# Performance work log

Hardware: AMD Instinct MI355X
Metric: run time of the kernel (lower is better)

The kernel has to match this reference:

```python
import jax, jax.numpy as jnp
import numpy as np

B, N, FEAT = 64, 1024, 3
HID, STATE, LAYERS, NTYPES = 64, 32, 2, 10


def setup_inputs() -> dict:
    key = jax.random.key(0)
    ks = jax.random.split(key, 16)
    s = 0.1
    return {
        "task_features": jax.random.normal(ks[0], (B, N, FEAT), jnp.float32),
        "task_types": jax.random.randint(ks[1], (B, N), 0, NTYPES, jnp.int32),
        "prev_state": jnp.zeros((B, STATE), jnp.float32),
        "enc_w1": jax.random.normal(ks[2], (HID, FEAT), jnp.float32) * s,
        "enc_b1": jnp.zeros((HID,), jnp.float32),
        "enc_w2": jax.random.normal(ks[3], (HID, HID), jnp.float32) * s,
        "enc_b2": jnp.zeros((HID,), jnp.float32),
        "contention": jax.random.normal(ks[4], (NTYPES, NTYPES), jnp.float32) * 0.1,
        "gnn_w": jax.random.normal(ks[5], (LAYERS, HID, HID), jnp.float32) * s,
        "gnn_b": jnp.zeros((LAYERS, HID), jnp.float32),
        "gru_w_ih": jax.random.normal(ks[6], (3 * STATE, HID), jnp.float32) * s,
        "gru_w_hh": jax.random.normal(ks[7], (3 * STATE, STATE), jnp.float32) * s,
        "gru_b_ih": jnp.zeros((3 * STATE,), jnp.float32),
        "gru_b_hh": jnp.zeros((3 * STATE,), jnp.float32),
        "head_w1": jax.random.normal(ks[8], (HID, HID + STATE), jnp.float32) * s,
        "head_b1": jnp.zeros((HID,), jnp.float32),
        "head_w2": jax.random.normal(ks[9], (1, HID), jnp.float32) * s,
        "head_b2": jnp.zeros((1,), jnp.float32),
    }


def _forward(task_features, task_types, prev_state, enc_w1, enc_b1, enc_w2, enc_b2,
             contention, gnn_w, gnn_b, gru_w_ih, gru_w_hh, gru_b_ih, gru_b_hh,
             head_w1, head_b1, head_w2, head_b2):
    # task encoder: Linear -> ReLU -> Linear
    emb = jax.nn.relu(task_features @ enc_w1.T + enc_b1) @ enc_w2.T + enc_b2  # (B,N,H)
    # interaction graph: type-pair gather + cosine similarity
    base = contention[task_types[:, :, None], task_types[:, None, :]]  # (B,N,N)
    nrm = emb / jnp.maximum(jnp.linalg.norm(emb, axis=-1, keepdims=True), 1e-12)
    sim = jnp.einsum("bnd,bmd->bnm", nrm, nrm)
    adjacency = jax.nn.sigmoid(base) * sim  # (B,N,N)
    # GNN layers: aggregate + linear + relu
    h = emb
    for l in range(LAYERS):
        agg = jnp.einsum("bnm,bmd->bnd", adjacency, h)
        h = jax.nn.relu((h + agg) @ gnn_w[l].T + gnn_b[l])
    ctx = h.mean(axis=1)  # (B,H)
    # GRUCell (torch semantics)
    gi = ctx @ gru_w_ih.T + gru_b_ih
    gh = prev_state @ gru_w_hh.T + gru_b_hh
    i_r, i_z, i_n = jnp.split(gi, 3, axis=-1)
    h_r, h_z, h_n = jnp.split(gh, 3, axis=-1)
    r = jax.nn.sigmoid(i_r + h_r)
    z = jax.nn.sigmoid(i_z + h_z)
    n = jnp.tanh(i_n + r * h_n)
    new_state = (1.0 - z) * n + z * prev_state  # (B,S)
    # latency head on [h, state]
    st = jnp.broadcast_to(new_state[:, None, :], (h.shape[0], h.shape[1], new_state.shape[-1]))
    combined = jnp.concatenate([h, st], axis=-1)
    lat = jax.nn.relu(combined @ head_w1.T + head_b1) @ head_w2.T + head_b2
    return lat[..., 0], new_state


def reference(task_features, task_types, prev_state, enc_w1, enc_b1, enc_w2, enc_b2,
              contention, gnn_w, gnn_b, gru_w_ih, gru_w_hh, gru_b_ih, gru_b_hh,
              head_w1, head_b1, head_w2, head_b2):
    return _forward(task_features, task_types, prev_state, enc_w1, enc_b1, enc_w2, enc_b2,
                    contention, gnn_w, gnn_b, gru_w_ih, gru_w_hh, gru_b_ih, gru_b_hh,
                    head_w1, head_b1, head_w2, head_b2)
```

## Files before the change

kernel.cpp:

```cpp
#include <hip/hip_runtime.h>
#include <math.h>

#define BB 64
#define NN 1024
#define HID 64
#define STATE 32
#define NTYPES 10
#define CAP 256
#define CAPE (CAP * 64)

typedef _Float16 f16;
typedef f16 f16x8 __attribute__((ext_vector_type(8)));
typedef f16 f16x4 __attribute__((ext_vector_type(4)));
typedef float f32x4 __attribute__((ext_vector_type(4)));

#define MFMA16(a, b, c) __builtin_amdgcn_mfma_f32_16x16x32_f16(a, b, c, 0, 0, 0)

__device__ __forceinline__ float sigm(float x) { return 1.f / (1.f + expf(-x)); }

__device__ __forceinline__ f16x8 cvt8(float4 a, float4 b) {
    f16x8 r;
    r[0] = (f16)a.x; r[1] = (f16)a.y; r[2] = (f16)a.z; r[3] = (f16)a.w;
    r[4] = (f16)b.x; r[5] = (f16)b.y; r[6] = (f16)b.z; r[7] = (f16)b.w;
    return r;
// ... 2 lines not shown
    union { f16 h[2]; unsigned u; } p;
    p.h[0] = a; p.h[1] = b;
    return p.u;
}

__device__ __forceinline__ void swz_load(const float* __restrict__ W, int K, int n,
                                         f16* dst, int tid) {
    for (int p = tid; p < n; p += 256) {
        int j = p & 7, ln = (p >> 3) & 63, nt = (p >> 9) & 3, ch = p >> 11;
        int k = ch * 32 + ((ln >> 4) << 3) + j;
        int o = nt * 16 + (ln & 15);
        dst[p] = (f16)W[o * K + k];
    }
}

__global__ __launch_bounds__(256) void k_encoder(
    const float* __restrict__ feat,
    const float* __restrict__ w1, const float* __restrict__ b1,
    const float* __restrict__ w2, const float* __restrict__ b2,
    const int* __restrict__ types, int* __restrict__ idx, int* __restrict__ cnt,
    f16* __restrict__ nrmp, float* __restrict__ sclp, float* __restrict__ ctx)
{
    __shared__ f16 w2s[4096];
    __shared__ f16 tmp[4][16 * 72];
    __shared__ float fbuf[4][48];
    __shared__ int pkbuf[64];
    int tid = threadIdx.x, wave = tid >> 6, lane = tid & 63;
    int l15 = lane & 15, quad = lane >> 4;
    if (tid < 64) {
        int row = blockIdx.x * 64 + tid;
        int b = row >> 10;
        int t = types[row];
        int bt = b * NTYPES + t;
        int pos = atomicAdd(&cnt[bt], 1);
        idx[bt * CAP + pos] = row & (NN - 1);
        pkbuf[tid] = bt * CAP + pos;
    }
    if (blockIdx.x < 16) ctx[blockIdx.x * 256 + tid] = 0.f;
    swz_load(w2, 64, 4096, w2s, tid);
    float w10 = w1[lane * 3], w11 = w1[lane * 3 + 1], w12 = w1[lane * 3 + 2], b1l = b1[lane];
    int tb = blockIdx.x * 64 + wave * 16;
    if (lane < 48) fbuf[wave][lane] = feat[tb * 3 + lane];
    __syncthreads();
    f16* tw = &tmp[wave][0];
#pragma unroll
    for (int r = 0; r < 16; ++r) {
        float x0 = fbuf[wave][r * 3], x1 = fbuf[wave][r * 3 + 1], x2 = fbuf[wave][r * 3 + 2];
        float hv = fmaxf(fmaf(w10, x0, fmaf(w11, x1, fmaf(w12, x2, b1l))), 0.f);
        tw[r * 72 + lane] = (f16)hv;
    }
    __builtin_amdgcn_sched_barrier(0);
    f16x8 a0 = *(const f16x8*)&tw[l15 * 72 + quad * 8];
    f16x8 a1 = *(const f16x8*)&tw[l15 * 72 + 32 + quad * 8];
    const f16x8* bf = (const f16x8*)w2s;
    f32x4 acc[4];
#pragma unroll
    for (int nt = 0; nt < 4; ++nt) {
        f32x4 c = {0.f, 0.f, 0.f, 0.f};
        c = MFMA16(a0, bf[(0 * 4 + nt) * 64 + lane], c);
        c = MFMA16(a1, bf[(1 * 4 + nt) * 64 + lane], c);
        acc[nt] = c;
    }
    float b2c[4];
#pragma unroll
    for (int nt = 0; nt < 4; ++nt) b2c[nt] = b2[nt * 16 + l15];
#pragma unroll
    for (int i = 0; i < 4; ++i) {
        float v[4]; float ss = 0.f;
#pragma unroll
        for (int nt = 0; nt < 4; ++nt) { v[nt] = acc[nt][i] + b2c[nt]; ss = fmaf(v[nt], v[nt], ss); }
        ss += __shfl_xor(ss, 1, 64); ss += __shfl_xor(ss, 2, 64);
        ss += __shfl_xor(ss, 4, 64); ss += __shfl_xor(ss, 8, 64);
        float nm = fmaxf(sqrtf(ss), 1e-12f);
        float rinv = 1.f / nm;
        int pk = pkbuf[wave * 16 + quad * 4 + i];
#pragma unroll
        for (int nt = 0; nt < 4; ++nt)
            nrmp[(size_t)pk * 64 + nt * 16 + l15] = (f16)(v[nt] * rinv);
        if (l15 == 0) sclp[pk] = nm;
    }
}

#define TSTR2 72
__global__ __launch_bounds__(256) void k_buildM0(
    const int* __restrict__ cnt, const f16* __restrict__ nrmp,
    const float* __restrict__ sclp, f16* __restrict__ M0)
{
    __shared__ f16 nT[64 * TSTR2];
    __shared__ f16 hT[64 * TSTR2];
    int i0 = blockIdx.x;
    int xcd = i0 & 7, kk = i0 >> 3;
    int b = xcd + 8 * (kk / NTYPES);
    int t = kk % NTYPES;
    int bt = b * NTYPES + t;
    int c = cnt[bt];
    int tid = threadIdx.x, wave = tid >> 6, lane = tid & 63;
    int l15 = lane & 15, quad = lane >> 4;
    int r = tid & 15, q4 = tid >> 4;
    const f16* nb = nrmp + (size_t)bt * CAPE;
    const float* sb = sclp + (size_t)bt * CAP;
    f32x4 acc[4] = {{0.f,0.f,0.f,0.f},{0.f,0.f,0.f,0.f},{0.f,0.f,0.f,0.f},{0.f,0.f,0.f,0.f}};
    for (int k0 = 0; k0 < c; k0 += 64) {
        __syncthreads();
        f16x4 a[4], g[4];
#pragma unroll
        for (int u = 0; u < 4; ++u) { a[u] = (f16x4){0,0,0,0}; g[u] = (f16x4){0,0,0,0}; }
#pragma unroll
        for (int u = 0; u < 4; ++u) {
            int mi = k0 + 4 * r + u;
            if (mi < c) {
                a[u] = *(const f16x4*)&nb[(size_t)mi * 64 + 4 * q4];
                f16 sm = (f16)sb[mi]; f16x4 sv = {sm, sm, sm, sm};
                g[u] = a[u] * sv;
            }
        }
#pragma unroll
        for (int i = 0; i < 4; ++i) {
            *(unsigned*)&nT[(4 * q4 + i) * TSTR2 + 4 * r]     = packh2(a[0][i], a[1][i]);
            *(unsigned*)&nT[(4 * q4 + i) * TSTR2 + 4 * r + 2] = packh2(a[2][i], a[3][i]);
            *(unsigned*)&hT[(4 * q4 + i) * TSTR2 + 4 * r]     = packh2(g[0][i], g[1][i]);
            *(unsigned*)&hT[(4 * q4 + i) * TSTR2 + 4 * r + 2] = packh2(g[2][i], g[3][i]);
        }
        __syncthreads();
        f16x8 af0 = *(const f16x8*)&nT[(wave * 16 + l15) * TSTR2 + quad * 8];
        f16x8 af1 = *(const f16x8*)&nT[(wave * 16 + l15) * TSTR2 + 32 + quad * 8];
#pragma unroll
        for (int nt = 0; nt < 4; ++nt) {
            f16x8 bf0 = *(const f16x8*)&hT[(nt * 16 + l15) * TSTR2 + quad * 8];
            f16x8 bf1 = *(const f16x8*)&hT[(nt * 16 + l15) * TSTR2 + 32 + quad * 8];
            acc[nt] = MFMA16(af0, bf0, acc[nt]);
            acc[nt] = MFMA16(af1, bf1, acc[nt]);
        }
    }
    f16* Mo = M0 + (size_t)bt * 4096;
#pragma unroll
    for (int nt = 0; nt < 4; ++nt)
#pragma unroll
        for (int i = 0; i < 4; ++i)
            Mo[(wave * 16 + quad * 4 + i) * 64 + nt * 16 + l15] = (f16)acc[nt][i];
}

__global__ __launch_bounds__(256) void k_gnn0_fused(
    const int* __restrict__ cnt, const float* __restrict__ cont,
    const f16* __restrict__ M, const f16* __restrict__ nrmp,
    const float* __restrict__ sclp,
    const float* __restrict__ gw, const float* __restrict__ gb,
    f16* __restrict__ h1p, f16* __restrict__ Mout)
{
    __shared__ f16 ds_[4096];
    __shared__ f16 gs[4096];
    __shared__ __align__(16) f16 nT[64 * TSTR2];
    __shared__ __align__(16) f16 hT[64 * TSTR2];
    int i0 = blockIdx.x;
    int xcd = i0 & 7, kk = i0 >> 3;
    int b = xcd + 8 * (kk / NTYPES);
    int t = kk % NTYPES;
    int bt = b * NTYPES + t;
    int c = cnt[bt];
    int tid = threadIdx.x, wave = tid >> 6, lane = tid & 63;
    int l15 = lane & 15, quad = lane >> 4;
    swz_load(gw, 64, 4096, gs, tid);
    float sg[NTYPES];
#pragma unroll
    for (int j = 0; j < NTYPES; ++j) sg[j] = sigm(cont[t * NTYPES + j]);
    float ca[16];
#pragma unroll
    for (int i = 0; i < 16; ++i) ca[i] = 0.f;
    const f16* Mb = M + (size_t)b * NTYPES * 4096;
#pragma unroll
    for (int j = 0; j < NTYPES; ++j) {
        const f16* Mr = Mb + j * 4096 + (wave * 16 + l15) * 64;
        f16x8 m0 = *(const f16x8*)&Mr[quad * 8];
        f16x8 m1 = *(const f16x8*)&Mr[32 + quad * 8];
        float sv = sg[j];
#pragma unroll
        for (int e = 0; e < 8; ++e) {
            ca[e]     = fmaf(sv, (float)m0[e], ca[e]);
            ca[8 + e] = fmaf(sv, (float)m1[e], ca[8 + e]);
        }
    }
    f16x8 ca0, ca1;
#pragma unroll
    for (int i = 0; i < 8; ++i) { ca0[i] = (f16)ca[i]; ca1[i] = (f16)ca[8 + i]; }
    __syncthreads();
    const f16x8* gbf = (const f16x8*)gs;
#pragma unroll
    for (int nt = 0; nt < 4; ++nt) {
        f32x4 dd = {0.f, 0.f, 0.f, 0.f};
        dd = MFMA16(ca0, gbf[(0 * 4 + nt) * 64 + lane], dd);
        dd = MFMA16(ca1, gbf[(1 * 4 + nt) * 64 + lane], dd);
#pragma unroll
        for (int i = 0; i < 4; ++i) {
            int d = wave * 16 + quad * 4 + i;
            int pos = (((d >> 5) * 4 + nt) * 64 + ((d >> 3) & 3) * 16 + l15) * 8 + (d & 7);
            ds_[pos] = (f16)dd[i];
        }
    }
    __syncthreads();
    float gbl[4];
#pragma unroll
    for (int nt = 0; nt < 4; ++nt) gbl[nt] = gb[nt * 16 + l15];
    const f16* nb = nrmp + (size_t)bt * CAPE;
    const float* sb = sclp + (size_t)bt * CAP;
    f16* hob = h1p + (size_t)bt * CAPE;
    const f16x8* dbf = (const f16x8*)ds_;
    f32x4 macc[4];
#pragma unroll
    for (int nt = 0; nt < 4; ++nt) macc[nt] = (f32x4){0.f, 0.f, 0.f, 0.f};
    int nchunk = (c + 63) >> 6;
    for (int ch = 0; ch < nchunk; ++ch) {
        int tb = ch * 64 + wave * 16;
        int rA = tb + l15;
        bool okA = rA < c;
        int rAc = okA ? rA : (c - 1);
        const f16* na = nb + (size_t)rAc * 64;
        f16x8 a0 = *(const f16x8*)&na[quad * 8];
        f16x8 a1 = *(const f16x8*)&na[32 + quad * 8];
        f32x4 acc1[4], acc2[4];
#pragma unroll
        for (int nt = 0; nt < 4; ++nt) {
            f32x4 c1 = {0.f, 0.f, 0.f, 0.f}, c2 = {0.f, 0.f, 0.f, 0.f};
            c1 = MFMA16(a0, dbf[(0 * 4 + nt) * 64 + lane], c1);
            c1 = MFMA16(a1, dbf[(1 * 4 + nt) * 64 + lane], c1);
            c2 = MFMA16(a0, gbf[(0 * 4 + nt) * 64 + lane], c2);
            c2 = MFMA16(a1, gbf[(1 * 4 + nt) * 64 + lane], c2);
            acc1[nt] = c1; acc2[nt] = c2;
        }
        f16x4 hv[4];
#pragma unroll
        for (int nt = 0; nt < 4; ++nt) hv[nt] = (f16x4){0, 0, 0, 0};
#pragma unroll
        for (int i = 0; i < 4; ++i) {
            int rr = tb + quad * 4 + i;
            if (rr < c) {
                float sm = sb[rr];
#pragma unroll
                for (int nt = 0; nt < 4; ++nt) {
                    float v = fmaxf(fmaf(sm, acc2[nt][i], acc1[nt][i]) + gbl[nt], 0.f);
                    f16 vh = (f16)v;
                    hob[(size_t)rr * 64 + nt * 16 + l15] = vh;
                    hv[nt][i] = vh;
                }
            }
        }
        f16x8 z8 = {0, 0, 0, 0, 0, 0, 0, 0};
        f16x8 s0 = okA ? a0 : z8;
        f16x8 s1 = okA ? a1 : z8;
#pragma unroll
        for (int j = 0; j < 8; ++j) {
            nT[(quad * 8 + j) * TSTR2 + wave * 16 + l15]      = s0[j];
            nT[(32 + quad * 8 + j) * TSTR2 + wave * 16 + l15] = s1[j];
        }
#pragma unroll
        for (int nt = 0; nt < 4; ++nt)
            *(f16x4*)&hT[(nt * 16 + l15) * TSTR2 + wave * 16 + quad * 4] = hv[nt];
        __syncthreads();
        f16x8 af0 = *(const f16x8*)&nT[(wave * 16 + l15) * TSTR2 + quad * 8];
        f16x8 af1 = *(const f16x8*)&nT[(wave * 16 + l15) * TSTR2 + 32 + quad * 8];
#pragma unroll
        for (int nt = 0; nt < 4; ++nt) {
            f16x8 bf0 = *(const f16x8*)&hT[(nt * 16 + l15) * TSTR2 + quad * 8];
            f16x8 bf1 = *(const f16x8*)&hT[(nt * 16 + l15) * TSTR2 + 32 + quad * 8];
            macc[nt] = MFMA16(af0, bf0, macc[nt]);
            macc[nt] = MFMA16(af1, bf1, macc[nt]);
        }
        __syncthreads();
    }
    f16* Mo = Mout + (size_t)bt * 4096;
#pragma unroll
    for (int nt = 0; nt < 4; ++nt)
#pragma unroll
        for (int i = 0; i < 4; ++i)
            Mo[(wave * 16 + quad * 4 + i) * 64 + nt * 16 + l15] = (f16)macc[nt][i];
}

__global__ __launch_bounds__(256) void k_gnn1(
    const int* __restrict__ cnt, const float* __restrict__ cont,
    const f16* __restrict__ M, const f16* __restrict__ nrmp,
    const f16* __restrict__ h1p,
    const float* __restrict__ gw, const float* __restrict__ gb,
    f16* __restrict__ h2p, float* __restrict__ ctx)
{
    __shared__ f16 ds_[4096];
    __shared__ f16 gs[4096];
    int i0 = blockIdx.x;
    int xcd = i0 & 7, kk = i0 >> 3;
    int b = xcd + 8 * (kk / NTYPES);
    int t = kk % NTYPES;
    int bt = b * NTYPES + t;
    int c = cnt[bt];
    if (c == 0) return;
    int tid = threadIdx.x, wave = tid >> 6, lane = tid & 63;
    int l15 = lane & 15, quad = lane >> 4;
    swz_load(gw, 64, 4096, gs, tid);
    float sg[NTYPES];
#pragma unroll
    for (int j = 0; j < NTYPES; ++j) sg[j] = sigm(cont[t * NTYPES + j]);
    float ca[16];
#pragma unroll
    for (int i = 0; i < 16; ++i) ca[i] = 0.f;
    const f16* Mb = M + (size_t)b * NTYPES * 4096;
#pragma unroll
    for (int j = 0; j < NTYPES; ++j) {
        const f16* Mr = Mb + j * 4096 + (wave * 16 + l15) * 64;
        f16x8 m0 = *(const f16x8*)&Mr[quad * 8];
        f16x8 m1 = *(const f16x8*)&Mr[32 + quad * 8];
        float sv = sg[j];
#pragma unroll
        for (int e = 0; e < 8; ++e) {
            ca[e]     = fmaf(sv, (float)m0[e], ca[e]);
            ca[8 + e] = fmaf(sv, (float)m1[e], ca[8 + e]);
        }
    }
    f16x8 ca0, ca1;
#pragma unroll
    for (int i = 0; i < 8; ++i) { ca0[i] = (f16)ca[i]; ca1[i] = (f16)ca[8 + i]; }
    __syncthreads();
    const f16x8* gbf = (const f16x8*)gs;
#pragma unroll
    for (int nt = 0; nt < 4; ++nt) {
        f32x4 dd = {0.f, 0.f, 0.f, 0.f};
        dd = MFMA16(ca0, gbf[(0 * 4 + nt) * 64 + lane], dd);
        dd = MFMA16(ca1, gbf[(1 * 4 + nt) * 64 + lane], dd);
#pragma unroll
        for (int i = 0; i < 4; ++i) {
            int d = wave * 16 + quad * 4 + i;
            int pos = (((d >> 5) * 4 + nt) * 64 + ((d >> 3) & 3) * 16 + l15) * 8 + (d & 7);
            ds_[pos] = (f16)dd[i];
        }
    }
    __syncthreads();
    float gbl[4];
#pragma unroll
    for (int nt = 0; nt < 4; ++nt) gbl[nt] = gb[nt * 16 + l15];
    const f16* nb = nrmp + (size_t)bt * CAPE;
    const f16* hb = h1p + (size_t)bt * CAPE;
    f16* hob = h2p + (size_t)bt * CAPE;
    const f16x8* dbf = (const f16x8*)ds_;
    float cacc[4] = {0.f, 0.f, 0.f, 0.f};
    for (int g = wave; g * 16 < c; g += 4) {
        int tb = g * 16;
        int rA = tb + l15; if (rA >= c) rA = c - 1;
        const f16* na = nb + (size_t)rA * 64;
        f16x8 a0 = *(const f16x8*)&na[quad * 8];
        f16x8 a1 = *(const f16x8*)&na[32 + quad * 8];
        const f16* ha = hb + (size_t)rA * 64;
        f16x8 h0 = *(const f16x8*)&ha[quad * 8];
        f16x8 h1 = *(const f16x8*)&ha[32 + quad * 8];
        f32x4 acc[4];
#pragma unroll
        for (int nt = 0; nt < 4; ++nt) {
            f32x4 cc = {0.f, 0.f, 0.f, 0.f};
            cc = MFMA16(a0, dbf[(0 * 4 + nt) * 64 + lane], cc);
            cc = MFMA16(a1, dbf[(1 * 4 + nt) * 64 + lane], cc);
            cc = MFMA16(h0, gbf[(0 * 4 + nt) * 64 + lane], cc);
            cc = MFMA16(h1, gbf[(1 * 4 + nt) * 64 + lane], cc);
            acc[nt] = cc;
        }
#pragma unroll
        for (int i = 0; i < 4; ++i) {
            int rr = tb + quad * 4 + i;
            if (rr < c) {
#pragma unroll
                for (int nt = 0; nt < 4; ++nt) {
                    float v = fmaxf(acc[nt][i] + gbl[nt], 0.f);
                    hob[(size_t)rr * 64 + nt * 16 + l15] = (f16)v;
                    cacc[nt] += v;
                }
            }
        }
    }
#pragma unroll
    for (int nt = 0; nt < 4; ++nt) {
        float sv = cacc[nt];
        sv += __shfl_xor(sv, 16, 64);
        sv += __shfl_xor(sv, 32, 64);
        if (quad == 0) atomicAdd(&ctx[b * HID + nt * 16 + l15], sv);
    }
}

__global__ __launch_bounds__(256) void k_head(
    const f16* __restrict__ h2p, const int* __restrict__ idx,
    const int* __restrict__ cnt, const float* __restrict__ ctx_sum,
    const float* __restrict__ prev,
    const float* __restrict__ w_ih, const float* __restrict__ w_hh,
    const float* __restrict__ b_ih, const float* __restrict__ b_hh,
    const float* __restrict__ hw1, const float* __restrict__ b1,
    const float* __restrict__ w2, const float* __restrict__ b2,
    float* __restrict__ lat, float* __restrict__ state_out)
{
    __shared__ f16 ws_[6144];
    __shared__ __align__(16) float st[STATE];
    __shared__ float cs[HID], ps[STATE], gis[96], ghs[96];
    int i0 = blockIdx.x;
    int xcd = i0 & 7, kk = i0 >> 3;
    int b = xcd + 8 * (kk / NTYPES);
    int t = kk % NTYPES;
    int bt = b * NTYPES + t;
    int c = cnt[bt];
    int tid = threadIdx.x, wave = tid >> 6, lane = tid & 63;
    int l15 = lane & 15, quad = lane >> 4;
    swz_load(hw1, 96, 6144, ws_, tid);
    if (tid < HID) cs[tid] = ctx_sum[b * HID + tid] * (1.f / NN);
    if (tid >= HID && tid < HID + STATE) ps[tid - HID] = prev[b * STATE + tid - HID];
    __syncthreads();
    if (tid < 96) {
        float gi = b_ih[tid];
#pragma unroll 8
        for (int k = 0; k < HID; ++k) gi = fmaf(w_ih[tid * HID + k], cs[k], gi);
        float gh = b_hh[tid];
#pragma unroll
        for (int k = 0; k < STATE; ++k) gh = fmaf(w_hh[tid * STATE + k], ps[k], gh);
        gis[tid] = gi; ghs[tid] = gh;
    }
    __syncthreads();
    if (tid < STATE) {
        float r = sigm(gis[tid] + ghs[tid]);
        float z = sigm(gis[32 + tid] + ghs[32 + tid]);
        float nn = tanhf(gis[64 + tid] + r * ghs[64 + tid]);
        float v = (1.f - z) * nn + z * ps[tid];
        st[tid] = v;
        if (t == 0) state_out[b * STATE + tid] = v;
    }
    __syncthreads();
    if (c == 0) return;
    float b1c[4], w2c[4];
#pragma unroll
    for (int nt = 0; nt < 4; ++nt) { b1c[nt] = b1[nt * 16 + l15]; w2c[nt] = w2[nt * 16 + l15]; }
    float b2v = b2[0];
    const float4* sp = (const float4*)st;
    f16x8 a2 = cvt8(sp[quad * 2], sp[quad * 2 + 1]);
    const f16x8* bf = (const f16x8*)ws_;
    const f16* hb = h2p + (size_t)bt * CAPE;
    const int* lst = idx + (size_t)bt * CAP;
    for (int g = wave; g * 16 < c; g += 4) {
        int tb = g * 16;
        int rA = tb + l15; if (rA >= c) rA = c - 1;
        const f16* ha = hb + (size_t)rA * 64;
        f16x8 a0 = *(const f16x8*)&ha[quad * 8];
        f16x8 a1 = *(const f16x8*)&ha[32 + quad * 8];
        f32x4 acc[4];
#pragma unroll
        for (int nt = 0; nt < 4; ++nt) {
            f32x4 cc = {0.f, 0.f, 0.f, 0.f};
// ... 36 lines not shown
    const float* b_ih   = (const float*)d_in[12];
    const float* b_hh   = (const float*)d_in[13];
    const float* hw1    = (const float*)d_in[14];
    const float* hb1    = (const float*)d_in[15];
    const float* hw2    = (const float*)d_in[16];
    const float* hb2    = (const float*)d_in[17];
    float* out = (float*)d_out;

    float* ws   = (float*)d_ws;
    f16*   nrmp = (f16*)ws;
    f16*   h1p  = (f16*)(ws + 5242880);
    f16*   h2p  = (f16*)(ws + 10485760);
    float* sclp = ws + 15728640;
    int*   idx  = (int*)(ws + 15892480);
    int*   cnt  = (int*)(ws + 16056320);
    f16*   M0   = (f16*)(ws + 16057344);
    f16*   M1   = (f16*)(ws + 17368064);
    float* ctx  = ws + 18678784;

    hipMemsetAsync(cnt, 0, BB * NTYPES * sizeof(int), stream);
    k_encoder<<<BB * NN / 64, 256, 0, stream>>>(feat, enc_w1, enc_b1, enc_w2, enc_b2,
                                                types, idx, cnt, nrmp, sclp, ctx);
    k_buildM0<<<BB * NTYPES, 256, 0, stream>>>(cnt, nrmp, sclp, M0);
    k_gnn0_fused<<<BB * NTYPES, 256, 0, stream>>>(cnt, cont, M0, nrmp, sclp,
                                                  gnn_w, gnn_b, h1p, M1);
    k_gnn1<<<BB * NTYPES, 256, 0, stream>>>(cnt, cont, M1, nrmp, h1p,
                                            gnn_w + 4096, gnn_b + HID, h2p, ctx);
    k_head<<<BB * NTYPES, 256, 0, stream>>>(h2p, idx, cnt, ctx, prev,
                                            w_ih, w_hh, b_ih, b_hh,
                                            hw1, hb1, hw2, hb2, out, out + BB * NN);
}
```

Measured before the change: 165.8 us.

## Merge five kernels into two persistent kernels with per-batch global barriers

Folds encoder, M0 build and GNN layer 0 into one kernel (k_front), and GNN layer 1 plus GRU and latency head into another (k_back). Stages are linked by per-batch atomic counters with spin-waits instead of kernel boundaries. This is meant to remove launch gaps and tail effects between the small kernels. The spin barriers rely on all 640 blocks being co-resident, which launch_bounds(256,3) on 256 CUs should allow, but a scheduling stall or deadlock risk is added.

```diff
diff --git a/kernel.cpp b/kernel.cpp
--- a/kernel.cpp
+++ b/kernel.cpp
@@ -40,395 +40,398 @@
     }
 }
 
-__global__ __launch_bounds__(256) void k_encoder(
+__device__ __forceinline__ void bar_signal(int* bar, int tid) {
+    if (tid == 0) { __threadfence(); atomicAdd(bar, 1); }
+}
+__device__ __forceinline__ void bar_wait(int* bar, int target, int tid) {
+    if (tid == 0) {
+        while (__hip_atomic_load(bar, __ATOMIC_ACQUIRE, __HIP_MEMORY_SCOPE_AGENT) < target)
+            __builtin_amdgcn_s_sleep(2);
+    }
+    __syncthreads();
+}
+
+#define TSTR2 72
+
+__global__ __launch_bounds__(256, 3) void k_front(
     const float* __restrict__ feat,
     const float* __restrict__ w1, const float* __restrict__ b1,
     const float* __restrict__ w2, const float* __restrict__ b2,
     const int* __restrict__ types, int* __restrict__ idx, int* __restrict__ cnt,
-    f16* __restrict__ nrmp, float* __restrict__ sclp, float* __restrict__ ctx)
+    f16* __restrict__ nrmp, float* __restrict__ sclp, float* __restrict__ ctx,
+    const float* __restrict__ cont, const float* __restrict__ gw0,
+    const float* __restrict__ gb0,
+    f16* __restrict__ M0, f16* __restrict__ M1, f16* __restrict__ h1p,
+    int* __restrict__ barE, int* __restrict__ bar0)
 {
-    __shared__ f16 w2s[4096];
-    __shared__ f16 tmp[4][16 * 72];
-    __shared__ float fbuf[4][48];
-    __shared__ int pkbuf[64];
-    int tid = threadIdx.x, wave = tid >> 6, lane = tid & 63;
-    int l15 = lane & 15, quad = lane >> 4;
-    if (tid < 64) {
-        int row = blockIdx.x * 64 + tid;
-        int b = row >> 10;
-        int t = types[row];
-        int bt = b * NTYPES + t;
-        int pos = atomicAdd(&cnt[bt], 1);
-        idx[bt * CAP + pos] = row & (NN - 1);
-        pkbuf[tid] = bt * CAP + pos;
-    }
-    if (blockIdx.x < 16) ctx[blockIdx.x * 256 + tid] = 0.f;
+    __shared__ __align__(16) unsigned char smem[34816];
+    f16* w2s = (f16*)smem;
+    f16* tmp = (f16*)(smem + 8192);
+    float* fb = (float*)(smem + 17408);
+    int* pkbuf = (int*)(smem + 18176);
+    f16* nT = (f16*)smem;
+    f16* hT = (f16*)(smem + 9216);
+    f16* gs = (f16*)(smem + 18432);
+    f16* ds_ = (f16*)(smem + 26624);
+
+    const int tid = threadIdx.x, wave = tid >> 6, lane = tid & 63;
+    const int l15 = lane & 15, quad = lane >> 4;
+    const int bid = blockIdx.x;
+
+    const int xcd = bid & 7, kk = bid >> 3;
+    const int rb = xcd + 8 * (kk / NTYPES);
+    const int rt = kk % NTYPES;
+    const int rbt = rb * NTYPES + rt;
+
+    swz_load(gw0, 64, 4096, gs, tid);
+    if (bid < 16) ctx[bid * 256 + tid] = 0.f;
+
     swz_load(w2, 64, 4096, w2s, tid);
     float w10 = w1[lane * 3], w11 = w1[lane * 3 + 1], w12 = w1[lane * 3 + 2], b1l = b1[lane];
-    int tb = blockIdx.x * 64 + wave * 16;
-    if (lane < 48) fbuf[wave][lane] = feat[tb * 3 + lane];
-    __syncthreads();
-    f16* tw = &tmp[wave][0];
-#pragma unroll
-    for (int r = 0; r < 16; ++r) {
-        float x0 = fbuf[wave][r * 3], x1 = fbuf[wave][r * 3 + 1], x2 = fbuf[wave][r * 3 + 2];
-        float hv = fmaxf(fmaf(w10, x0, fmaf(w11, x1, fmaf(w12, x2, b1l))), 0.f);
-        tw[r * 72 + lane] = (f16)hv;
-    }
-    __builtin_amdgcn_sched_barrier(0);
-    f16x8 a0 = *(const f16x8*)&tw[l15 * 72 + quad * 8];
-    f16x8 a1 = *(const f16x8*)&tw[l15 * 72 + 32 + quad * 8];
-    const f16x8* bf = (const f16x8*)w2s;
-    f32x4 acc[4];
-#pragma unroll
-    for (int nt = 0; nt < 4; ++nt) {
-        f32x4 c = {0.f, 0.f, 0.f, 0.f};
-        c = MFMA16(a0, bf[(0 * 4 + nt) * 64 + lane], c);
-        c = MFMA16(a1, bf[(1 * 4 + nt) * 64 + lane], c);
-        acc[nt] = c;
-    }
     float b2c[4];
 #pragma unroll
     for (int nt = 0; nt < 4; ++nt) b2c[nt] = b2[nt * 16 + l15];
-#pragma unroll
-    for (int i = 0; i < 4; ++i) {
-        float v[4]; float ss = 0.f;
-#pragma unroll
-        for (int nt = 0; nt < 4; ++nt) { v[nt] = acc[nt][i] + b2c[nt]; ss = fmaf(v[nt], v[nt], ss); }
-        ss += __shfl_xor(ss, 1, 64); ss += __shfl_xor(ss, 2, 64);
-        ss += __shfl_xor(ss, 4, 64); ss += __shfl_xor(ss, 8, 64);
-        float nm = fmaxf(sqrtf(ss), 1e-12f);
-        float rinv = 1.f / nm;
-        int pk = pkbuf[wave * 16 + quad * 4 + i];
+    f16* tw = &tmp[wave * (16 * 72)];
+    float* fw = &fb[wave * 48];
+    const f16x8* wbf = (const f16x8*)w2s;
+    for (int tile = bid; tile < BB * NN / 64; tile += 640) {
+        int tbatch = tile >> 4;
+        if (tid < 64) {
+            int row = tile * 64 + tid;
+            int t = types[row];
+            int bt = tbatch * NTYPES + t;
+            int pos = atomicAdd(&cnt[bt], 1);
+            idx[bt * CAP + pos] = row & (NN - 1);
+            pkbuf[tid] = bt * CAP + pos;
+        }
+        int tb = tile * 64 + wave * 16;
+        if (lane < 48) fw[lane] = feat[tb * 3 + lane];
+        __syncthreads();
+#pragma unroll
+        for (int r = 0; r < 16; ++r) {
+            float x0 = fw[r * 3], x1 = fw[r * 3 + 1], x2 = fw[r * 3 + 2];
+            float hv = fmaxf(fmaf(w10, x0, fmaf(w11, x1, fmaf(w12, x2, b1l))), 0.f);
+            tw[r * 72 + lane] = (f16)hv;
+        }
+        __builtin_amdgcn_sched_barrier(0);
+        f16x8 a0 = *(const f16x8*)&tw[l15 * 72 + quad * 8];
+        f16x8 a1 = *(const f16x8*)&tw[l15 * 72 + 32 + quad * 8];
+        f32x4 acc[4];
+#pragma unroll
+        for (int nt = 0; nt < 4; ++nt) {
+            f32x4 c = {0.f, 0.f, 0.f, 0.f};
+            c = MFMA16(a0, wbf[(0 * 4 + nt) * 64 + lane], c);
+            c = MFMA16(a1, wbf[(1 * 4 + nt) * 64 + lane], c);
+            acc[nt] = c;
+        }
+#pragma unroll
+        for (int i = 0; i < 4; ++i) {
+            float v[4]; float ss = 0.f;
+#pragma unroll
+            for (int nt = 0; nt < 4; ++nt) { v[nt] = acc[nt][i] + b2c[nt]; ss = fmaf(v[nt], v[nt], ss); }
+            ss += __shfl_xor(ss, 1, 64); ss += __shfl_xor(ss, 2, 64);
+            ss += __shfl_xor(ss, 4, 64); ss += __shfl_xor(ss, 8, 64);
+            float nm = fmaxf(sqrtf(ss), 1e-12f);
+            float rinv = 1.f / nm;
+            int pk = pkbuf[wave * 16 + quad * 4 + i];
+#pragma unroll
+            for (int nt = 0; nt < 4; ++nt)
+                nrmp[(size_t)pk * 64 + nt * 16 + l15] = (f16)(v[nt] * rinv);
+            if (l15 == 0) sclp[pk] = nm;
+        }
+        __syncthreads();
+        bar_signal(&barE[tbatch], tid);
+    }
+
+    bar_wait(&barE[rb], 16, tid);
+    int c = cnt[rbt];
+
+    {
+        int r = tid & 15, q4 = tid >> 4;
+        const f16* nb = nrmp + (size_t)rbt * CAPE;
+        const float* sb = sclp + (size_t)rbt * CAP;
+        f32x4 acc[4] = {{0.f,0.f,0.f,0.f},{0.f,0.f,0.f,0.f},{0.f,0.f,0.f,0.f},{0.f,0.f,0.f,0.f}};
+        for (int k0 = 0; k0 < c; k0 += 64) {
+            __syncthreads();
+            f16x4 a[4], g[4];
+#pragma unroll
+            for (int u = 0; u < 4; ++u) { a[u] = (f16x4){0,0,0,0}; g[u] = (f16x4){0,0,0,0}; }
+#pragma unroll
+            for (int u = 0; u < 4; ++u) {
+                int mi = k0 + 4 * r + u;
+                if (mi < c) {
+                    a[u] = *(const f16x4*)&nb[(size_t)mi * 64 + 4 * q4];
+                    f16 sm = (f16)sb[mi]; f16x4 sv = {sm, sm, sm, sm};
+                    g[u] = a[u] * sv;
+                }
+            }
+#pragma unroll
+            for (int i = 0; i < 4; ++i) {
+                *(unsigned*)&nT[(4 * q4 + i) * TSTR2 + 4 * r]     = packh2(a[0][i], a[1][i]);
+                *(unsigned*)&nT[(4 * q4 + i) * TSTR2 + 4 * r + 2] = packh2(a[2][i], a[3][i]);
+                *(unsigned*)&hT[(4 * q4 + i) * TSTR2 + 4 * r]     = packh2(g[0][i], g[1][i]);
+                *(unsigned*)&hT[(4 * q4 + i) * TSTR2 + 4 * r + 2] = packh2(g[2][i], g[3][i]);
+            }
+            __syncthreads();
+            f16x8 af0 = *(const f16x8*)&nT[(wave * 16 + l15) * TSTR2 + quad * 8];
+            f16x8 af1 = *(const f16x8*)&nT[(wave * 16 + l15) * TSTR2 + 32 + quad * 8];
+#pragma unroll
+            for (int nt = 0; nt < 4; ++nt) {
+                f16x8 bf0 = *(const f16x8*)&hT[(nt * 16 + l15) * TSTR2 + quad * 8];
+                f16x8 bf1 = *(const f16x8*)&hT[(nt * 16 + l15) * TSTR2 + 32 + quad * 8];
+                acc[nt] = MFMA16(af0, bf0, acc[nt]);
+                acc[nt] = MFMA16(af1, bf1, acc[nt]);
+            }
+        }
+        f16* Mo = M0 + (size_t)rbt * 4096;
 #pragma unroll
         for (int nt = 0; nt < 4; ++nt)
-            nrmp[(size_t)pk * 64 + nt * 16 + l15] = (f16)(v[nt] * rinv);
-        if (l15 == 0) sclp[pk] = nm;
-    }
-}
-
-#define TSTR2 72
-__global__ __launch_bounds__(256) void k_buildM0(
-    const int* __restrict__ cnt, const f16* __restrict__ nrmp,
-    const float* __restrict__ sclp, f16* __restrict__ M0)
-{
-    __shared__ f16 nT[64 * TSTR2];
-    __shared__ f16 hT[64 * TSTR2];
-    int i0 = blockIdx.x;
-    int xcd = i0 & 7, kk = i0 >> 3;
-    int b = xcd + 8 * (kk / NTYPES);
-    int t = kk % NTYPES;
-    int bt = b * NTYPES + t;
-    int c = cnt[bt];
-    int tid = threadIdx.x, wave = tid >> 6, lane = tid & 63;
-    int l15 = lane & 15, quad = lane >> 4;
-    int r = tid & 15, q4 = tid >> 4;
-    const f16* nb = nrmp + (size_t)bt * CAPE;
-    const float* sb = sclp + (size_t)bt * CAP;
-    f32x4 acc[4] = {{0.f,0.f,0.f,0.f},{0.f,0.f,0.f,0.f},{0.f,0.f,0.f,0.f},{0.f,0.f,0.f,0.f}};
-    for (int k0 = 0; k0 < c; k0 += 64) {
+#pragma unroll
+            for (int i = 0; i < 4; ++i)
+                Mo[(wave * 16 + quad * 4 + i) * 64 + nt * 16 + l15] = (f16)acc[nt][i];
+    }
+    __syncthreads();
+    bar_signal(&bar0[rb], tid);
+    bar_wait(&bar0[rb], 10, tid);
+
+    {
+        float sg[NTYPES];
+#pragma unroll
+        for (int j = 0; j < NTYPES; ++j) sg[j] = sigm(cont[rt * NTYPES + j]);
+        float ca[16];
+#pragma unroll
+        for (int i = 0; i < 16; ++i) ca[i] = 0.f;
+        const f16* Mb = M0 + (size_t)rb * NTYPES * 4096;
+#pragma unroll
+        for (int j = 0; j < NTYPES; ++j) {
+            const f16* Mr = Mb + j * 4096 + (wave * 16 + l15) * 64;
+            f16x8 m0 = *(const f16x8*)&Mr[quad * 8];
+            f16x8 m1 = *(const f16x8*)&Mr[32 + quad * 8];
+            float sv = sg[j];
+#pragma unroll
+            for (int e = 0; e < 8; ++e) {
+                ca[e]     = fmaf(sv, (float)m0[e], ca[e]);
+                ca[8 + e] = fmaf(sv, (float)m1[e], ca[8 + e]);
+            }
+        }
+        f16x8 ca0, ca1;
+#pragma unroll
+        for (int i = 0; i < 8; ++i) { ca0[i] = (f16)ca[i]; ca1[i] = (f16)ca[8 + i]; }
+        const f16x8* gbf = (const f16x8*)gs;
+#pragma unroll
+        for (int nt = 0; nt < 4; ++nt) {
+            f32x4 dd = {0.f, 0.f, 0.f, 0.f};
+            dd = MFMA16(ca0, gbf[(0 * 4 + nt) * 64 + lane], dd);
+            dd = MFMA16(ca1, gbf[(1 * 4 + nt) * 64 + lane], dd);
+#pragma unroll
+            for (int i = 0; i < 4; ++i) {
+                int d = wave * 16 + quad * 4 + i;
+                int pos = (((d >> 5) * 4 + nt) * 64 + ((d >> 3) & 3) * 16 + l15) * 8 + (d & 7);
+                ds_[pos] = (f16)dd[i];
+            }
+        }
         __syncthreads();
-        f16x4 a[4], g[4];
-#pragma unroll
-        for (int u = 0; u < 4; ++u) { a[u] = (f16x4){0,0,0,0}; g[u] = (f16x4){0,0,0,0}; }
-#pragma unroll
-        for (int u = 0; u < 4; ++u) {
-            int mi = k0 + 4 * r + u;
-            if (mi < c) {
-                a[u] = *(const f16x4*)&nb[(size_t)mi * 64 + 4 * q4];
-                f16 sm = (f16)sb[mi]; f16x4 sv = {sm, sm, sm, sm};
-                g[u] = a[u] * sv;
-            }
-        }
-#pragma unroll
-        for (int i = 0; i < 4; ++i) {
-            *(unsigned*)&nT[(4 * q4 + i) * TSTR2 + 4 * r]     = packh2(a[0][i], a[1][i]);
-            *(unsigned*)&nT[(4 * q4 + i) * TSTR2 + 4 * r + 2] = packh2(a[2][i], a[3][i]);
-            *(unsigned*)&hT[(4 * q4 + i) * TSTR2 + 4 * r]     = packh2(g[0][i], g[1][i]);
-            *(unsigned*)&hT[(4 * q4 + i) * TSTR2 + 4 * r + 2] = packh2(g[2][i], g[3][i]);
-        }
-        __syncthreads();
-        f16x8 af0 = *(const f16x8*)&nT[(wave * 16 + l15) * TSTR2 + quad * 8];
-        f16x8 af1 = *(const f16x8*)&nT[(wave * 16 + l15) * TSTR2 + 32 + quad * 8];
-#pragma unroll
-        for (int nt = 0; nt < 4; ++nt) {
-            f16x8 bf0 = *(const f16x8*)&hT[(nt * 16 + l15) * TSTR2 + quad * 8];
-            f16x8 bf1 = *(const f16x8*)&hT[(nt * 16 + l15) * TSTR2 + 32 + quad * 8];
-            acc[nt] = MFMA16(af0, bf0, acc[nt]);
-            acc[nt] = MFMA16(af1, bf1, acc[nt]);
-        }
-    }
-    f16* Mo = M0 + (size_t)bt * 4096;
-#pragma unroll
-    for (int nt = 0; nt < 4; ++nt)
-#pragma unroll
-        for (int i = 0; i < 4; ++i)
-            Mo[(wave * 16 + quad * 4 + i) * 64 + nt * 16 + l15] = (f16)acc[nt][i];
-}
-
-__global__ __launch_bounds__(256) void k_gnn0_fused(
+        float gbl[4];
+#pragma unroll
+        for (int nt = 0; nt < 4; ++nt) gbl[nt] = gb0[nt * 16 + l15];
+        const f16* nb = nrmp + (size_t)rbt * CAPE;
+        const float* sb = sclp + (size_t)rbt * CAP;
+        f16* hob = h1p + (size_t)rbt * CAPE;
+        const f16x8* dbf = (const f16x8*)ds_;
+        f32x4 macc[4];
+#pragma unroll
+        for (int nt = 0; nt < 4; ++nt) macc[nt] = (f32x4){0.f, 0.f, 0.f, 0.f};
+        int nchunk = (c + 63) >> 6;
+        for (int ch = 0; ch < nchunk; ++ch) {
+            int tb = ch * 64 + wave * 16;
+            int rA = tb + l15;
+            bool okA = rA < c;
+            int rAc = okA ? rA : (c - 1);
+            const f16* na = nb + (size_t)rAc * 64;
+            f16x8 a0 = *(const f16x8*)&na[quad * 8];
+            f16x8 a1 = *(const f16x8*)&na[32 + quad * 8];
+            f32x4 acc1[4], acc2[4];
+#pragma unroll
+            for (int nt = 0; nt < 4; ++nt) {
+                f32x4 c1 = {0.f, 0.f, 0.f, 0.f}, c2 = {0.f, 0.f, 0.f, 0.f};
+                c1 = MFMA16(a0, dbf[(0 * 4 + nt) * 64 + lane], c1);
+                c1 = MFMA16(a1, dbf[(1 * 4 + nt) * 64 + lane], c1);
+                c2 = MFMA16(a0, gbf[(0 * 4 + nt) * 64 + lane], c2);
+                c2 = MFMA16(a1, gbf[(1 * 4 + nt) * 64 + lane], c2);
+                acc1[nt] = c1; acc2[nt] = c2;
+            }
+            f16x4 hv[4];
+#pragma unroll
+            for (int nt = 0; nt < 4; ++nt) hv[nt] = (f16x4){0, 0, 0, 0};
+#pragma unroll
+            for (int i = 0; i < 4; ++i) {
+                int rr = tb + quad * 4 + i;
+                if (rr < c) {
+                    float sm = sb[rr];
+#pragma unroll
+                    for (int nt = 0; nt < 4; ++nt) {
+                        float v = fmaxf(fmaf(sm, acc2[nt][i], acc1[nt][i]) + gbl[nt], 0.f);
+                        f16 vh = (f16)v;
+                        hob[(size_t)rr * 64 + nt * 16 + l15] = vh;
+                        hv[nt][i] = vh;
+                    }
+                }
+            }
+            f16x8 z8 = {0, 0, 0, 0, 0, 0, 0, 0};
+            f16x8 s0 = okA ? a0 : z8;
+            f16x8 s1 = okA ? a1 : z8;
+#pragma unroll
+            for (int j = 0; j < 8; ++j) {
+                nT[(quad * 8 + j) * TSTR2 + wave * 16 + l15]      = s0[j];
+                nT[(32 + quad * 8 + j) * TSTR2 + wave * 16 + l15] = s1[j];
+            }
+#pragma unroll
+            for (int nt = 0; nt < 4; ++nt)
+                *(f16x4*)&hT[(nt * 16 + l15) * TSTR2 + wave * 16 + quad * 4] = hv[nt];
+            __syncthreads();
+            f16x8 af0 = *(const f16x8*)&nT[(wave * 16 + l15) * TSTR2 + quad * 8];
+            f16x8 af1 = *(const f16x8*)&nT[(wave * 16 + l15) * TSTR2 + 32 + quad * 8];
+#pragma unroll
+            for (int nt = 0; nt < 4; ++nt) {
+                f16x8 bf0 = *(const f16x8*)&hT[(nt * 16 + l15) * TSTR2 + quad * 8];
+                f16x8 bf1 = *(const f16x8*)&hT[(nt * 16 + l15) * TSTR2 + 32 + quad * 8];
+                macc[nt] = MFMA16(af0, bf0, macc[nt]);
+                macc[nt] = MFMA16(af1, bf1, macc[nt]);
+            }
+            __syncthreads();
+        }
+        f16* Mo = M1 + (size_t)rbt * 4096;
+#pragma unroll
+        for (int nt = 0; nt < 4; ++nt)
+#pragma unroll
+            for (int i = 0; i < 4; ++i)
+                Mo[(wave * 16 + quad * 4 + i) * 64 + nt * 16 + l15] = (f16)macc[nt][i];
+    }
+}
+
+__global__ __launch_bounds__(256, 3) void k_back(
     const int* __restrict__ cnt, const float* __restrict__ cont,
-    const f16* __restrict__ M, const f16* __restrict__ nrmp,
-    const float* __restrict__ sclp,
-    const float* __restrict__ gw, const float* __restrict__ gb,
-    f16* __restrict__ h1p, f16* __restrict__ Mout)
+    const f16* __restrict__ M1, const f16* __restrict__ nrmp,
+    const f16* __restrict__ h1p,
+    const float* __restrict__ gw1, const float* __restrict__ gb1,
+    f16* __restrict__ h2p, float* __restrict__ ctx,
+    const int* __restrict__ idx, const float* __restrict__ prev,
+    const float* __restrict__ w_ih, const float* __restrict__ w_hh,
+    const float* __restrict__ b_ih, const float* __restrict__ b_hh,
+    const float* __restrict__ hw1, const float* __restrict__ hb1,
+    const float* __restrict__ hw2, const float* __restrict__ hb2,
+    float* __restrict__ lat, float* __restrict__ state_out,
+    int* __restrict__ bar1)
 {
     __shared__ f16 ds_[4096];
     __shared__ f16 gs[4096];
-    __shared__ __align__(16) f16 nT[64 * TSTR2];
-    __shared__ __align__(16) f16 hT[64 * TSTR2];
-    int i0 = blockIdx.x;
-    int xcd = i0 & 7, kk = i0 >> 3;
-    int b = xcd + 8 * (kk / NTYPES);
-    int t = kk % NTYPES;
-    int bt = b * NTYPES + t;
-    int c = cnt[bt];
-    int tid = threadIdx.x, wave = tid >> 6, lane = tid & 63;
-    int l15 = lane & 15, quad = lane >> 4;
-    swz_load(gw, 64, 4096, gs, tid);
-    float sg[NTYPES];
-#pragma unroll
-    for (int j = 0; j < NTYPES; ++j) sg[j] = sigm(cont[t * NTYPES + j]);
-    float ca[16];
-#pragma unroll
-    for (int i = 0; i < 16; ++i) ca[i] = 0.f;
-    const f16* Mb = M + (size_t)b * NTYPES * 4096;
-#pragma unroll
-    for (int j = 0; j < NTYPES; ++j) {
-        const f16* Mr = Mb + j * 4096 + (wave * 16 + l15) * 64;
-        f16x8 m0 = *(const f16x8*)&Mr[quad * 8];
-        f16x8 m1 = *(const f16x8*)&Mr[32 + quad * 8];
-        float sv = sg[j];
-#pragma unroll
-        for (int e = 0; e < 8; ++e) {
-            ca[e]     = fmaf(sv, (float)m0[e], ca[e]);
-            ca[8 + e] = fmaf(sv, (float)m1[e], ca[8 + e]);
-        }
-    }
-    f16x8 ca0, ca1;
-#pragma unroll
-    for (int i = 0; i < 8; ++i) { ca0[i] = (f16)ca[i]; ca1[i] = (f16)ca[8 + i]; }
-    __syncthreads();
-    const f16x8* gbf = (const f16x8*)gs;
-#pragma unroll
-    for (int nt = 0; nt < 4; ++nt) {
-        f32x4 dd = {0.f, 0.f, 0.f, 0.f};
-        dd = MFMA16(ca0, gbf[(0 * 4 + nt) * 64 + lane], dd);
-        dd = MFMA16(ca1, gbf[(1 * 4 + nt) * 64 + lane], dd);
-#pragma unroll
-        for (int i = 0; i < 4; ++i) {
-            int d = wave * 16 + quad * 4 + i;
-            int pos = (((d >> 5) * 4 + nt) * 64 + ((d >> 3) & 3) * 16 + l15) * 8 + (d & 7);
-            ds_[pos] = (f16)dd[i];
-        }
-    }
-    __syncthreads();
-    float gbl[4];
-#pragma unroll
-    for (int nt = 0; nt < 4; ++nt) gbl[nt] = gb[nt * 16 + l15];
-    const f16* nb = nrmp + (size_t)bt * CAPE;
-    const float* sb = sclp + (size_t)bt * CAP;
-    f16* hob = h1p + (size_t)bt * CAPE;
-    const f16x8* dbf = (const f16x8*)ds_;
-    f32x4 macc[4];
-#pragma unroll
-    for (int nt = 0; nt < 4; ++nt) macc[nt] = (f32x4){0.f, 0.f, 0.f, 0.f};
-    int nchunk = (c + 63) >> 6;
-    for (int ch = 0; ch < nchunk; ++ch) {
-        int tb = ch * 64 + wave * 16;
-        int rA = tb + l15;
-        bool okA = rA < c;
-        int rAc = okA ? rA : (c - 1);
-        const f16* na = nb + (size_t)rAc * 64;
-        f16x8 a0 = *(const f16x8*)&na[quad * 8];
-        f16x8 a1 = *(const f16x8*)&na[32 + quad * 8];
-        f32x4 acc1[4], acc2[4];
-#pragma unroll
-        for (int nt = 0; nt < 4; ++nt) {
-            f32x4 c1 = {0.f, 0.f, 0.f, 0.f}, c2 = {0.f, 0.f, 0.f, 0.f};
-            c1 = MFMA16(a0, dbf[(0 * 4 + nt) * 64 + lane], c1);
-            c1 = MFMA16(a1, dbf[(1 * 4 + nt) * 64 + lane], c1);
-            c2 = MFMA16(a0, gbf[(0 * 4 + nt) * 64 + lane], c2);
-            c2 = MFMA16(a1, gbf[(1 * 4 + nt) * 64 + lane], c2);
-            acc1[nt] = c1; acc2[nt] = c2;
-        }
-        f16x4 hv[4];
-#pragma unroll
-        for (int nt = 0; nt < 4; ++nt) hv[nt] = (f16x4){0, 0, 0, 0};
-#pragma unroll
-        for (int i = 0; i < 4; ++i) {
-            int rr = tb + quad * 4 + i;
-            if (rr < c) {
-                float sm = sb[rr];
-#pragma unroll
-                for (int nt = 0; nt < 4; ++nt) {
-                    float v = fmaxf(fmaf(sm, acc2[nt][i], acc1[nt][i]) + gbl[nt], 0.f);
-                    f16 vh = (f16)v;
-                    hob[(size_t)rr * 64 + nt * 16 + l15] = vh;
-                    hv[nt][i] = vh;
-                }
-            }
-        }
-        f16x8 z8 = {0, 0, 0, 0, 0, 0, 0, 0};
-        f16x8 s0 = okA ? a0 : z8;
-        f16x8 s1 = okA ? a1 : z8;
-#pragma unroll
-        for (int j = 0; j < 8; ++j) {
-            nT[(quad * 8 + j) * TSTR2 + wave * 16 + l15]      = s0[j];
-            nT[(32 + quad * 8 + j) * TSTR2 + wave * 16 + l15] = s1[j];
-        }
-#pragma unroll
-        for (int nt = 0; nt < 4; ++nt)
-            *(f16x4*)&hT[(nt * 16 + l15) * TSTR2 + wave * 16 + quad * 4] = hv[nt];
-        __syncthreads();
-        f16x8 af0 = *(const f16x8*)&nT[(wave * 16 + l15) * TSTR2 + quad * 8];
-        f16x8 af1 = *(const f16x8*)&nT[(wave * 16 + l15) * TSTR2 + 32 + quad * 8];
-#pragma unroll
-        for (int nt = 0; nt < 4; ++nt) {
-            f16x8 bf0 = *(const f16x8*)&hT[(nt * 16 + l15) * TSTR2 + quad * 8];
-            f16x8 bf1 = *(const f16x8*)&hT[(nt * 16 + l15) * TSTR2 + 32 + quad * 8];
-            macc[nt] = MFMA16(af0, bf0, macc[nt]);
-            macc[nt] = MFMA16(af1, bf1, macc[nt]);
-        }
-        __syncthreads();
-    }
-    f16* Mo = Mout + (size_t)bt * 4096;
-#pragma unroll
-    for (int nt = 0; nt < 4; ++nt)
-#pragma unroll
-        for (int i = 0; i < 4; ++i)
-            Mo[(wave * 16 + quad * 4 + i) * 64 + nt * 16 + l15] = (f16)macc[nt][i];
-}
-
-__global__ __launch_bounds__(256) void k_gnn1(
-    const int* __restrict__ cnt, const float* __restrict__ cont,
-    const f16* __restrict__ M, const f16* __restrict__ nrmp,
-    const f16* __restrict__ h1p,
-    const float* __restrict__ gw, const float* __restrict__ gb,
-    f16* __restrict__ h2p, float* __restrict__ ctx)
-{
-    __shared__ f16 ds_[4096];
-    __shared__ f16 gs[4096];
-    int i0 = blockIdx.x;
-    int xcd = i0 & 7, kk = i0 >> 3;
-    int b = xcd + 8 * (kk / NTYPES);
-    int t = kk % NTYPES;
-    int bt = b * NTYPES + t;
-    int c = cnt[bt];
-    if (c == 0) return;
-    int tid = threadIdx.x, wave = tid >> 6, lane = tid & 63;
-    int l15 = lane & 15, quad = lane >> 4;
-    swz_load(gw, 64, 4096, gs, tid);
-    float sg[NTYPES];
-#pragma unroll
-    for (int j = 0; j < NTYPES; ++j) sg[j] = sigm(cont[t * NTYPES + j]);
-    float ca[16];
-#pragma unroll
-    for (int i = 0; i < 16; ++i) ca[i] = 0.f;
-    const f16* Mb = M + (size_t)b * NTYPES * 4096;
-#pragma unroll
-    for (int j = 0; j < NTYPES; ++j) {
-        const f16* Mr = Mb + j * 4096 + (wave * 16 + l15) * 64;
-        f16x8 m0 = *(const f16x8*)&Mr[quad * 8];
-        f16x8 m1 = *(const f16x8*)&Mr[32 + quad * 8];
-        float sv = sg[j];
-#pragma unroll
-        for (int e = 0; e < 8; ++e) {
-            ca[e]     = fmaf(sv, (float)m0[e], ca[e]);
-            ca[8 + e] = fmaf(sv, (float)m1[e], ca[8 + e]);
-        }
-    }
-    f16x8 ca0, ca1;
-#pragma unroll
-    for (int i = 0; i < 8; ++i) { ca0[i] = (f16)ca[i]; ca1[i] = (f16)ca[8 + i]; }
-    __syncthreads();
-    const f16x8* gbf = (const f16x8*)gs;
-#pragma unroll
-    for (int nt = 0; nt < 4; ++nt) {
-        f32x4 dd = {0.f, 0.f, 0.f, 0.f};
-        dd = MFMA16(ca0, gbf[(0 * 4 + nt) * 64 + lane], dd);
-        dd = MFMA16(ca1, gbf[(1 * 4 + nt) * 64 + lane], dd);
-#pragma unroll
-        for (int i = 0; i < 4; ++i) {
-            int d = wave * 16 + quad * 4 + i;
-            int pos = (((d >> 5) * 4 + nt) * 64 + ((d >> 3) & 3) * 16 + l15) * 8 + (d & 7);
-            ds_[pos] = (f16)dd[i];
-        }
-    }
-    __syncthreads();
-    float gbl[4];
-#pragma unroll
-    for (int nt = 0; nt < 4; ++nt) gbl[nt] = gb[nt * 16 + l15];
-    const f16* nb = nrmp + (size_t)bt * CAPE;
-    const f16* hb = h1p + (size_t)bt * CAPE;
-    f16* hob = h2p + (size_t)bt * CAPE;
-    const f16x8* dbf = (const f16x8*)ds_;
-    float cacc[4] = {0.f, 0.f, 0.f, 0.f};
-    for (int g = wave; g * 16 < c; g += 4) {
-        int tb = g * 16;
-        int rA = tb + l15; if (rA >= c) rA = c - 1;
-        const f16* na = nb + (size_t)rA * 64;
-        f16x8 a0 = *(const f16x8*)&na[quad * 8];
-        f16x8 a1 = *(const f16x8*)&na[32 + quad * 8];
-        const f16* ha = hb + (size_t)rA * 64;
-        f16x8 h0 = *(const f16x8*)&ha[quad * 8];
-        f16x8 h1 = *(const f16x8*)&ha[32 + quad * 8];
-        f32x4 acc[4];
-#pragma unroll
-        for (int nt = 0; nt < 4; ++nt) {
-            f32x4 cc = {0.f, 0.f, 0.f, 0.f};
-            cc = MFMA16(a0, dbf[(0 * 4 + nt) * 64 + lane], cc);
-            cc = MFMA16(a1, dbf[(1 * 4 + nt) * 64 + lane], cc);
-            cc = MFMA16(h0, gbf[(0 * 4 + nt) * 64 + lane], cc);
-            cc = MFMA16(h1, gbf[(1 * 4 + nt) * 64 + lane], cc);
-            acc[nt] = cc;
-        }
-#pragma unroll
-        for (int i = 0; i < 4; ++i) {
-            int rr = tb + quad * 4 + i;
-            if (rr < c) {
-#pragma unroll
-                for (int nt = 0; nt < 4; ++nt) {
-                    float v = fmaxf(acc[nt][i] + gbl[nt], 0.f);
-                    hob[(size_t)rr * 64 + nt * 16 + l15] = (f16)v;
-                    cacc[nt] += v;
-                }
-            }
-        }
-    }
-#pragma unroll
-    for (int nt = 0; nt < 4; ++nt) {
-        float sv = cacc[nt];
-        sv += __shfl_xor(sv, 16, 64);
-        sv += __shfl_xor(sv, 32, 64);
-        if (quad == 0) atomicAdd(&ctx[b * HID + nt * 16 + l15], sv);
-    }
-}
-
-__global__ __launch_bounds__(256) void k_head(
-    const f16* __restrict__ h2p, const int* __restrict__ idx,
-    const int* __restrict__ cnt, const float* __restrict__ ctx_sum,
-    const float* __restrict__ prev,
-    const float* __restrict__ w_ih, const float* __restrict__ w_hh,
-    const float* __restrict__ b_ih, const float* __restrict__ b_hh,
-    const float* __restrict__ hw1, const float* __restrict__ b1,
-    const float* __restrict__ w2, const float* __restrict__ b2,
-    float* __restrict__ lat, float* __restrict__ state_out)
-{
     __shared__ f16 ws_[6144];
     __shared__ __align__(16) float st[STATE];
     __shared__ float cs[HID], ps[STATE], gis[96], ghs[96];
-    int i0 = blockIdx.x;
-    int xcd = i0 & 7, kk = i0 >> 3;
-    int b = xcd + 8 * (kk / NTYPES);
-    int t = kk % NTYPES;
-    int bt = b * NTYPES + t;
-    int c = cnt[bt];
-    int tid = threadIdx.x, wave = tid >> 6, lane = tid & 63;
-    int l15 = lane & 15, quad = lane >> 4;
+    const int tid = threadIdx.x, wave = tid >> 6, lane = tid & 63;
+    const int l15 = lane & 15, quad = lane >> 4;
+    const int bid = blockIdx.x;
+    const int xcd = bid & 7, kk = bid >> 3;
+    const int b = xcd + 8 * (kk / NTYPES);
+    const int t = kk % NTYPES;
+    const int bt = b * NTYPES + t;
+    const int c = cnt[bt];
+
+    swz_load(gw1, 64, 4096, gs, tid);
     swz_load(hw1, 96, 6144, ws_, tid);
-    if (tid < HID) cs[tid] = ctx_sum[b * HID + tid] * (1.f / NN);
     if (tid >= HID && tid < HID + STATE) ps[tid - HID] = prev[b * STATE + tid - HID];
+    __syncthreads();
+
+    if (c > 0) {
+        float sg[NTYPES];
+#pragma unroll
+        for (int j = 0; j < NTYPES; ++j) sg[j] = sigm(cont[t * NTYPES + j]);
+        float ca[16];
+#pragma unroll
+        for (int i = 0; i < 16; ++i) ca[i] = 0.f;
+        const f16* Mb = M1 + (size_t)b * NTYPES * 4096;
+#pragma unroll
+        for (int j = 0; j < NTYPES; ++j) {
+            const f16* Mr = Mb + j * 4096 + (wave * 16 + l15) * 64;
+            f16x8 m0 = *(const f16x8*)&Mr[quad * 8];
+            f16x8 m1 = *(const f16x8*)&Mr[32 + quad * 8];
+            float sv = sg[j];
+#pragma unroll
+            for (int e = 0; e < 8; ++e) {
+                ca[e]     = fmaf(sv, (float)m0[e], ca[e]);
+                ca[8 + e] = fmaf(sv, (float)m1[e], ca[8 + e]);
+            }
+        }
+        f16x8 ca0, ca1;
+#pragma unroll
+        for (int i = 0; i < 8; ++i) { ca0[i] = (f16)ca[i]; ca1[i] = (f16)ca[8 + i]; }
+        const f16x8* gbf = (const f16x8*)gs;
+#pragma unroll
+        for (int nt = 0; nt < 4; ++nt) {
+            f32x4 dd = {0.f, 0.f, 0.f, 0.f};
+            dd = MFMA16(ca0, gbf[(0 * 4 + nt) * 64 + lane], dd);
+            dd = MFMA16(ca1, gbf[(1 * 4 + nt) * 64 + lane], dd);
+#pragma unroll
+            for (int i = 0; i < 4; ++i) {
+                int d = wave * 16 + quad * 4 + i;
+                int pos = (((d >> 5) * 4 + nt) * 64 + ((d >> 3) & 3) * 16 + l15) * 8 + (d & 7);
+                ds_[pos] = (f16)dd[i];
+            }
+        }
+        __syncthreads();
+        float gbl[4];
+#pragma unroll
+        for (int nt = 0; nt < 4; ++nt) gbl[nt] = gb1[nt * 16 + l15];
+        const f16* nb = nrmp + (size_t)bt * CAPE;
+        const f16* hb = h1p + (size_t)bt * CAPE;
+        f16* hob = h2p + (size_t)bt * CAPE;
+        const f16x8* dbf = (const f16x8*)ds_;
+        float cacc[4] = {0.f, 0.f, 0.f, 0.f};
+        for (int g = wave; g * 16 < c; g += 4) {
+            int tb = g * 16;
+            int rA = tb + l15; if (rA >= c) rA = c - 1;
+            const f16* na = nb + (size_t)rA * 64;
+            f16x8 a0 = *(const f16x8*)&na[quad * 8];
+            f16x8 a1 = *(const f16x8*)&na[32 + quad * 8];
+            const f16* ha = hb + (size_t)rA * 64;
+            f16x8 h0 = *(const f16x8*)&ha[quad * 8];
+            f16x8 h1 = *(const f16x8*)&ha[32 + quad * 8];
+            f32x4 acc[4];
+#pragma unroll
+            for (int nt = 0; nt < 4; ++nt) {
+                f32x4 cc = {0.f, 0.f, 0.f, 0.f};
+                cc = MFMA16(a0, dbf[(0 * 4 + nt) * 64 + lane], cc);
+                cc = MFMA16(a1, dbf[(1 * 4 + nt) * 64 + lane], cc);
+                cc = MFMA16(h0, gbf[(0 * 4 + nt) * 64 + lane], cc);
+                cc = MFMA16(h1, gbf[(1 * 4 + nt) * 64 + lane], cc);
+                acc[nt] = cc;
+            }
+#pragma unroll
+            for (int i = 0; i < 4; ++i) {
+                int rr = tb + quad * 4 + i;
+                if (rr < c) {
+#pragma unroll
+                    for (int nt = 0; nt < 4; ++nt) {
+                        float v = fmaxf(acc[nt][i] + gbl[nt], 0.f);
+                        hob[(size_t)rr * 64 + nt * 16 + l15] = (f16)v;
+                        cacc[nt] += v;
+                    }
+                }
+            }
+        }
+#pragma unroll
+        for (int nt = 0; nt < 4; ++nt) {
+            float sv = cacc[nt];
+            sv += __shfl_xor(sv, 16, 64);
+            sv += __shfl_xor(sv, 32, 64);
+            if (quad == 0) atomicAdd(&ctx[b * HID + nt * 16 + l15], sv);
+        }
+    }
+    __syncthreads();
+    bar_signal(&bar1[b], tid);
+    bar_wait(&bar1[b], 10, tid);
+
+    if (tid < HID) cs[tid] = ctx[b * HID + tid] * (1.f / NN);
     __syncthreads();
     if (tid < 96) {
         float gi = b_ih[tid];
@@ -452,8 +455,8 @@
     if (c == 0) return;
     float b1c[4], w2c[4];
 #pragma unroll
-    for (int nt = 0; nt < 4; ++nt) { b1c[nt] = b1[nt * 16 + l15]; w2c[nt] = w2[nt * 16 + l15]; }
-    float b2v = b2[0];
+    for (int nt = 0; nt < 4; ++nt) { b1c[nt] = hb1[nt * 16 + l15]; w2c[nt] = hw2[nt * 16 + l15]; }
+    float b2v = hb2[0];
     const float4* sp = (const float4*)st;
     f16x8 a2 = cvt8(sp[quad * 2], sp[quad * 2 + 1]);
     const f16x8* bf = (const f16x8*)ws_;
@@ -520,19 +523,21 @@
     float* sclp = ws + 15728640;
     int*   idx  = (int*)(ws + 15892480);
     int*   cnt  = (int*)(ws + 16056320);
+    int*   barE = cnt + 640;
+    int*   bar0 = barE + 64;
+    int*   bar1 = bar0 + 64;
     f16*   M0   = (f16*)(ws + 16057344);
     f16*   M1   = (f16*)(ws + 17368064);
     float* ctx  = ws + 18678784;
 
-    hipMemsetAsync(cnt, 0, BB * NTYPES * sizeof(int), stream);
-    k_encoder<<<BB * NN / 64, 256, 0, stream>>>(feat, enc_w1, enc_b1, enc_w2, enc_b2,
-                                                types, idx, cnt, nrmp, sclp, ctx);
-    k_buildM0<<<BB * NTYPES, 256, 0, stream>>>(cnt, nrmp, sclp, M0);
-    k_gnn0_fused<<<BB * NTYPES, 256, 0, stream>>>(cnt, cont, M0, nrmp, sclp,
-                                                  gnn_w, gnn_b, h1p, M1);
-    k_gnn1<<<BB * NTYPES, 256, 0, stream>>>(cnt, cont, M1, nrmp, h1p,
-                                            gnn_w + 4096, gnn_b + HID, h2p, ctx);
-    k_head<<<BB * NTYPES, 256, 0, stream>>>(h2p, idx, cnt, ctx, prev,
-                                            w_ih, w_hh, b_ih, b_hh,
-                                            hw1, hb1, hw2, hb2, out, out + BB * NN);
-}
+    hipMemsetAsync(cnt, 0, 832 * sizeof(int), stream);
+    k_front<<<BB * NTYPES, 256, 0, stream>>>(feat, enc_w1, enc_b1, enc_w2, enc_b2,
+                                             types, idx, cnt, nrmp, sclp, ctx,
+                                             cont, gnn_w, gnn_b, M0, M1, h1p,
+                                             barE, bar0);
+    k_back<<<BB * NTYPES, 256, 0, stream>>>(cnt, cont, M1, nrmp, h1p,
+                                            gnn_w + 4096, gnn_b + HID, h2p, ctx,
+                                            idx, prev, w_ih, w_hh, b_ih, b_hh,
+                                            hw1, hb1, hw2, hb2,
+                                            out, out + BB * NN, bar1);
+}
```

After: 355.0 us. 2.14x slower.
